# Kernel tuning notes

Measured on AMD Instinct MI355X. Metric: run time of the kernel, lower is better.

The kernel has to match this reference:

```python
import jax, jax.numpy as jnp
import numpy as np

INF = 1000000000000.0
V, H, E, B, T, S, NUM_OOV = 32000, 512, 300, 32, 32, 400, 50


def setup_inputs() -> dict:
    key = jax.random.key(0)
    ks = jax.random.split(key, 20)
    sc = 0.02
    inp = {
        'trg_seq_embedded': jax.random.normal(ks[0], (B, T, E), jnp.float32),
        'ext_src_seq': jax.random.randint(ks[1], (B, S), 0, V + NUM_OOV, jnp.int32),
        'init_states': jax.random.normal(ks[2], (1, B, H), jnp.float32),
        'encoder_outputs': jax.random.normal(ks[3], (B, S, H), jnp.float32),
        'encoder_mask': jax.random.randint(ks[4], (B, S), 0, 2, jnp.int32),
        # parameters (PyTorch Linear convention: y = x @ W.T + b)
        'W_enc': sc * jax.random.normal(ks[5], (H, H), jnp.float32),
        'b_enc': jnp.zeros((H,), jnp.float32),
        'W_red': sc * jax.random.normal(ks[6], (E, E + H), jnp.float32),
        'b_red': jnp.zeros((E,), jnp.float32),
        'W_ih': sc * jax.random.normal(ks[7], (4 * H, E), jnp.float32),
        'W_hh': sc * jax.random.normal(ks[8], (4 * H, H), jnp.float32),
        'b_ih': jnp.zeros((4 * H,), jnp.float32),
        'b_hh': jnp.zeros((4 * H,), jnp.float32),
        'W_cat': sc * jax.random.normal(ks[9], (H, 2 * H), jnp.float32),
        'b_cat': jnp.zeros((H,), jnp.float32),
        'W_log': sc * jax.random.normal(ks[10], (V, H), jnp.float32),
        'b_log': jnp.zeros((V,), jnp.float32),
    }
    return inp


def decoder_forward(trg_seq_embedded, init_states, encoder_outputs,
                    W_enc, b_enc, W_red, b_red, W_ih, W_hh, b_ih, b_hh,
                    W_cat, b_cat, W_log, b_log, ext_src_seq, encoder_mask):
    batch, max_len, _ = trg_seq_embedded.shape
    src_len = encoder_outputs.shape[1]
    hidden = encoder_outputs.shape[-1]
    memories = encoder_outputs @ W_enc.T + b_enc            # [B,S,H]
    mask0 = (encoder_mask == 0)                              # [B,S]
    bidx = jnp.arange(batch)[:, None]                        # [B,1]

    h0 = init_states[0]
    c0 = init_states[0]
    ctx0 = jnp.zeros((batch, hidden), trg_seq_embedded.dtype)
    cov0 = jnp.zeros((batch, src_len), trg_seq_embedded.dtype)

    def step(carry, emb_t):
        h, c, prev_ctx, cov = carry
        x = jnp.concatenate([emb_t, prev_ctx], axis=-1) @ W_red.T + b_red
        gates = x @ W_ih.T + b_ih + h @ W_hh.T + b_hh
        i, f, g, o = jnp.split(gates, 4, axis=-1)
        c_new = jax.nn.sigmoid(f) * c + jax.nn.sigmoid(i) * jnp.tanh(g)
        h_new = jax.nn.sigmoid(o) * jnp.tanh(c_new)
        energy = jnp.einsum('bh,bsh->bs', h_new, memories)
        energy = jnp.where(mask0, -INF, energy)
        attn = jax.nn.softmax(energy, axis=-1)
        ctx = jnp.einsum('bs,bsh->bh', attn, memories)
        logit_in = jnp.tanh(jnp.concatenate([h_new, ctx], axis=-1) @ W_cat.T + b_cat)
        logit = logit_in @ W_log.T + b_log                   # [B,V]
        ext = jnp.concatenate([logit, jnp.zeros((batch, NUM_OOV), logit.dtype)], axis=1)
        out = jnp.full_like(ext, -INF).at[bidx, ext_src_seq].max(energy)
        out = jnp.where(out == -INF, 0.0, out)
        logit_ext = ext + out
        logit_ext = jnp.where(logit_ext == 0.0, -INF, logit_ext)
        return (h_new, c_new, ctx, cov + attn), (logit_ext, attn, cov, energy)

    _, (logits, attns, covs, energies) = jax.lax.scan(
        step, (h0, c0, ctx0, cov0), jnp.swapaxes(trg_seq_embedded, 0, 1))
    return logits, attns, covs, energies


def reference(trg_seq_embedded, ext_src_seq, init_states, encoder_outputs, encoder_mask,
              W_enc, b_enc, W_red, b_red, W_ih, W_hh, b_ih, b_hh,
              W_cat, b_cat, W_log, b_log):
    return decoder_forward(trg_seq_embedded, init_states, encoder_outputs,
                           W_enc, b_enc, W_red, b_red, W_ih, W_hh, b_ih, b_hh,
                           W_cat, b_cat, W_log, b_log, ext_src_seq, encoder_mask)
```

## Files before the change

### kernel.cpp

```cpp
#include <hip/hip_runtime.h>
#include <hip/hip_bf16.h>

#define INF_F 1000000000000.0f

typedef __attribute__((ext_vector_type(8))) short bfrag8;
typedef __attribute__((ext_vector_type(4))) float facc4;
typedef __attribute__((ext_vector_type(4))) short short4v;

__device__ __forceinline__ float sigf(float x){ return 1.0f/(1.0f + expf(-x)); }
__device__ __forceinline__ short f2bf(float f){
  __hip_bfloat16 h = __float2bfloat16(f);
  return *reinterpret_cast<short*>(&h);
}
__device__ __forceinline__ float bf2f(short s){
  unsigned u = ((unsigned)(unsigned short)s) << 16;
  return *reinterpret_cast<float*>(&u);
}

#define OFF_LOG 0ull
#define OFF_A   32819200ull
#define OFF_C   33228800ull
#define OFF_E   33638400ull

__global__ __launch_bounds__(256) void k_init(const float* __restrict__ init_s,
    float* __restrict__ hbuf, float* __restrict__ c0, float* __restrict__ ctxb,
    float* __restrict__ cov) {
  int i = blockIdx.x*256 + threadIdx.x;
  if (i < 32*512) { float v = init_s[i]; hbuf[i]=v; c0[i]=v; ctxb[i]=0.0f; }
  if (i < 32*400) cov[i] = 0.0f;
}

__global__ __launch_bounds__(256) void k_bcombo(const float* __restrict__ W_ih,
    const float* __restrict__ b_red, const float* __restrict__ b_ih,
    const float* __restrict__ b_hh, float* __restrict__ bcomb) {
  int j = blockIdx.x*256 + threadIdx.x;
  if (j >= 2048) return;
  float acc = b_ih[j] + b_hh[j];
  for (int m=0;m<300;m++) acc += W_ih[j*300+m]*b_red[m];
  bcomb[j] = acc;
}

__global__ __launch_bounds__(256) void k_wcombo(const float* __restrict__ W_ih,
    const float* __restrict__ W_red, float* __restrict__ Wct) {
  __shared__ float As[16][68];
  __shared__ float Bs[16][68];
  int tid = threadIdx.x;
  int m0 = blockIdx.y*64, n0 = blockIdx.x*64;
  int rl = tid>>2, kq = (tid&3)*4;
  int kl = tid>>4, c4 = (tid&15)*4;
  int tx = tid&15, ty = tid>>4;
  float acc[4][4]={};
  for (int kk=0;kk<300;kk+=16){
    #pragma unroll
    for (int q=0;q<4;q++){
      int kg = kk+kq+q;
      As[kq+q][rl] = (kg<300) ? W_ih[(size_t)(m0+rl)*300 + kg] : 0.0f;
    }
    #pragma unroll
    for (int q=0;q<4;q++){
      int c = n0 + c4 + q;
      Bs[kl][c4+q] = (kk+kl<300 && c<812) ? W_red[(size_t)(kk+kl)*812 + c] : 0.0f;
    }
    __syncthreads();
    #pragma unroll
    for (int k=0;k<16;k++){
      const float* ap=&As[k][ty*4]; const float* bp=&Bs[k][tx*4];
      #pragma unroll
      for (int i=0;i<4;i++)
        #pragma unroll
        for (int j=0;j<4;j++) acc[i][j] += ap[i]*bp[j];
    }
    __syncthreads();
  }
  #pragma unroll
  for (int i=0;i<4;i++)
    #pragma unroll
    for (int j=0;j<4;j++){
      int row = m0+ty*4+i, col = n0+tx*4+j;
      if (col<812) Wct[(size_t)row*812 + col] = acc[i][j];
    }
}

__global__ __launch_bounds__(256) void k_gemb(const float* __restrict__ trg,
    const float* __restrict__ Wct, const float* __restrict__ bcomb,
    float* __restrict__ Gemb) {
  __shared__ float As[16][68];
  __shared__ float Bs[16][68];
  int tid = threadIdx.x;
  int m0 = blockIdx.y*64, n0 = blockIdx.x*64;
  int rl = tid>>2, kq = (tid&3)*4;
  int tx = tid&15, ty = tid>>4;
  float acc[4][4]={};
  int r = m0 + rl;
  const float* arow = trg + (size_t)(r&31)*9600 + (size_t)(r>>5)*300;
  for (int kk=0;kk<300;kk+=16){
    #pragma unroll
    for (int q=0;q<4;q++){
      int kg = kk+kq+q;
      As[kq+q][rl] = (kg<300) ? arow[kg] : 0.0f;
      Bs[kq+q][rl] = (kg<300) ? Wct[(size_t)(n0+rl)*812 + kg] : 0.0f;
    }
    __syncthreads();
    #pragma unroll
    for (int k=0;k<16;k++){
      const float* ap=&As[k][ty*4]; const float* bp=&Bs[k][tx*4];
      #pragma unroll
      for (int i=0;i<4;i++)
        #pragma unroll
        for (int j=0;j<4;j++) acc[i][j] += ap[i]*bp[j];
    }
    __syncthreads();
  }
  #pragma unroll
  for (int i=0;i<4;i++)
    #pragma unroll
    for (int j=0;j<4;j++){
      int rr = m0+ty*4+i, col = n0+tx*4+j;
      Gemb[(size_t)rr*2048 + col] = acc[i][j] + bcomb[col];
    }
}

__global__ __launch_bounds__(256) void k_wgpack(const float* __restrict__ Wct,
    const float* __restrict__ W_hh, float* __restrict__ Wg) {
  int idx = blockIdx.x*256 + threadIdx.x;
  if (idx >= 1024*2048) return;
  int k = idx >> 11, j = idx & 2047;
  Wg[idx] = (k < 512) ? Wct[(size_t)j*812 + 300 + k] : W_hh[(size_t)j*512 + (k-512)];
}

__global__ __launch_bounds__(256) void k_convsplit(const float* __restrict__ enc,
    const float* __restrict__ W_enc, short* __restrict__ ehi, short* __restrict__ elo,
    short* __restrict__ whi, short* __restrict__ wlo) {
  int i4 = blockIdx.x*256 + threadIdx.x;
  const float* src; short* dhi; short* dlo; size_t off;
  if (i4 < 1638400) { src = enc;   dhi = ehi; dlo = elo; off = (size_t)i4*4; }
  else { int j4 = i4 - 1638400; if (j4 >= 65536) return;
         src = W_enc; dhi = whi; dlo = wlo; off = (size_t)j4*4; }
  float4 v = *(const float4*)(src + off);
  float f[4] = {v.x, v.y, v.z, v.w};
  short4v h, l;
  #pragma unroll
  for (int q=0;q<4;q++){
    short hb = f2bf(f[q]);
    float r = f[q] - bf2f(hb);
    h[q] = hb; l[q] = f2bf(r);
  }
  *(short4v*)(dhi + off) = h;
  *(short4v*)(dlo + off) = l;
}

__device__ __forceinline__ int lds_off(int row, int slot) {
  return (row<<6) + (((slot ^ ((row>>1)&3))&3)<<4);
}

__global__ __launch_bounds__(256) void k_memories(const short* __restrict__ Ahg,
    const short* __restrict__ Alg, const short* __restrict__ Bhg,
    const short* __restrict__ Blg, const float* __restrict__ bias,
    float* __restrict__ mem) {
  __shared__ short Ah[4096];
  __shared__ short Al[4096];
  __shared__ short Bh[4096];
  __shared__ short Bl[4096];
  int tid = threadIdx.x;
  int m0 = blockIdx.x*128, n0 = blockIdx.y*128;
  int w = tid>>6, lane = tid&63;
  int wr = w>>1, wc = w&1;
  int lr = lane&15, kg2 = lane>>4;

  int srow = tid>>1;
  int ss   = (tid&1)*2;
  const short* gah = Ahg + (size_t)(m0+srow)*512 + ss*8;
  const short* gal = Alg + (size_t)(m0+srow)*512 + ss*8;
  const short* gbh = Bhg + (size_t)(n0+srow)*512 + ss*8;
  const short* gbl = Blg + (size_t)(n0+srow)*512 + ss*8;
  int wo0 = lds_off(srow, ss), wo1 = lds_off(srow, ss+1);

  int raoff[4], rboff[4];
  #pragma unroll
  for (int q=0;q<4;q++){
    raoff[q] = lds_off(wr*64 + q*16 + lr, kg2);
    rboff[q] = lds_off(wc*64 + q*16 + lr, kg2);
  }

  facc4 acc[4][4] = {};
  bfrag8 rah0 = *(const bfrag8*)(gah);
  bfrag8 rah1 = *(const bfrag8*)(gah+8);
  bfrag8 ral0 = *(const bfrag8*)(gal);
  bfrag8 ral1 = *(const bfrag8*)(gal+8);
  bfrag8 rbh0 = *(const bfrag8*)(gbh);
  bfrag8 rbh1 = *(const bfrag8*)(gbh+8);
  bfrag8 rbl0 = *(const bfrag8*)(gbl);
  bfrag8 rbl1 = *(const bfrag8*)(gbl+8);

  for (int i=0;i<16;i++){
    __syncthreads();
    *(bfrag8*)((char*)Ah + wo0) = rah0;
    *(bfrag8*)((char*)Ah + wo1) = rah1;
    *(bfrag8*)((char*)Al + wo0) = ral0;
    *(bfrag8*)((char*)Al + wo1) = ral1;
    *(bfrag8*)((char*)Bh + wo0) = rbh0;
    *(bfrag8*)((char*)Bh + wo1) = rbh1;
    *(bfrag8*)((char*)Bl + wo0) = rbl0;
    *(bfrag8*)((char*)Bl + wo1) = rbl1;
    __syncthreads();
    if (i<15){
      gah += 32; gal += 32; gbh += 32; gbl += 32;
      rah0 = *(const bfrag8*)(gah);
      rah1 = *(const bfrag8*)(gah+8);
      ral0 = *(const bfrag8*)(gal);
      ral1 = *(const bfrag8*)(gal+8);
      rbh0 = *(const bfrag8*)(gbh);
      rbh1 = *(const bfrag8*)(gbh+8);
      rbl0 = *(const bfrag8*)(gbl);
      rbl1 = *(const bfrag8*)(gbl+8);
    }
    bfrag8 afh[4], afl[4], bfh[4], bfl[4];
    #pragma unroll
    for (int q=0;q<4;q++){
      afh[q] = *(const bfrag8*)((char*)Ah + raoff[q]);
      afl[q] = *(const bfrag8*)((char*)Al + raoff[q]);
      bfh[q] = *(const bfrag8*)((char*)Bh + rboff[q]);
      bfl[q] = *(const bfrag8*)((char*)Bl + rboff[q]);
    }
    #pragma unroll
    for (int mi=0;mi<4;mi++)
      #pragma unroll
      for (int ni=0;ni<4;ni++){
        acc[mi][ni] = __builtin_amdgcn_mfma_f32_16x16x32_bf16(afl[mi], bfh[ni], acc[mi][ni], 0,0,0);
        acc[mi][ni] = __builtin_amdgcn_mfma_f32_16x16x32_bf16(afh[mi], bfl[ni], acc[mi][ni], 0,0,0);
        acc[mi][ni] = __builtin_amdgcn_mfma_f32_16x16x32_bf16(afh[mi], bfh[ni], acc[mi][ni], 0,0,0);
      }
  }

  #pragma unroll
  for (int mi=0;mi<4;mi++){
    int row = m0 + wr*64 + mi*16 + kg2*4;
    #pragma unroll
    for (int ni=0;ni<4;ni++){
      int col = n0 + wc*64 + ni*16 + lr;
      float bl = bias[col];
      #pragma unroll
      for (int q=0;q<4;q++)
        mem[(size_t)(row+q)*512 + col] = acc[mi][ni][q] + bl;
    }
  }
}

__global__ __launch_bounds__(256) void k_wlogconv(const float* __restrict__ W_log,
    __hip_bfloat16* __restrict__ wlb, const float* __restrict__ W_cat,
    short* __restrict__ wcatb) {
  int i4 = blockIdx.x*256 + threadIdx.x;
  if (i4 < 4096000) {
    const float4 v = *(const float4*)(W_log + (size_t)i4*4);
    size_t o = (size_t)i4*4;
    wlb[o+0] = __float2bfloat16(v.x); wlb[o+1] = __float2bfloat16(v.y);
    wlb[o+2] = __float2bfloat16(v.z); wlb[o+3] = __float2bfloat16(v.w);
  } else {
    int j4 = i4 - 4096000;
    if (j4 >= 131072) return;
    const float4 v = *(const float4*)(W_cat + (size_t)j4*4);
    short4v s;
    s[0]=f2bf(v.x); s[1]=f2bf(v.y); s[2]=f2bf(v.z); s[3]=f2bf(v.w);
    *(short4v*)(wcatb + (size_t)j4*4) = s;
  }
}

__global__ __launch_bounds__(512) void k_gates(const float* __restrict__ ctxb,
    const float* __restrict__ hbuf, const float* __restrict__ Wg,
    float* __restrict__ partials) {
  __shared__ float yh_s[64][32];
  int ks = blockIdx.x;
  int rc = blockIdx.y;
  int tid = threadIdx.x;
  const float* side = (ks < 8) ? ctxb : hbuf;
  int kbase = (ks & 7) * 64;
  {
    int b_l = tid & 31, kq0 = (tid >> 5) * 4;
    const float* src = side + (size_t)b_l*512 + kbase + kq0;
    float4 v = *(const float4*)src;
    yh_s[kq0+0][b_l]=v.x; yh_s[kq0+1][b_l]=v.y;
    yh_s[kq0+2][b_l]=v.z; yh_s[kq0+3][b_l]=v.w;
  }
  __syncthreads();
  int tr = tid & 63, bg = tid >> 6;
  int row0 = rc*128 + tr*2;
  float acc[2][4] = {};
  const float* wp = Wg + (size_t)(ks*64)*2048 + row0;
  #pragma unroll 8
  for (int k=0;k<64;k++){
    float2 w = *(const float2*)(wp + (size_t)k*2048);
    float4 y = *(const float4*)&yh_s[k][bg*4];
    acc[0][0]+=w.x*y.x; acc[0][1]+=w.x*y.y; acc[0][2]+=w.x*y.z; acc[0][3]+=w.x*y.w;
    acc[1][0]+=w.y*y.x; acc[1][1]+=w.y*y.y; acc[1][2]+=w.y*y.z; acc[1][3]+=w.y*y.w;
  }
  #pragma unroll
  for (int j=0;j<4;j++){
    float2 o; o.x=acc[0][j]; o.y=acc[1][j];
    *(float2*)(partials + (size_t)(ks*32 + bg*4 + j)*2048 + row0) = o;
  }
}

__global__ __launch_bounds__(512) void k_lstm_energy(const float* __restrict__ part,
    const float* __restrict__ Gemb,
    const float* __restrict__ c_in, float* __restrict__ c_out,
    float* __restrict__ hbuf, short* __restrict__ licat,
    const float* __restrict__ mem, const int* __restrict__ emask,
    float* __restrict__ out, int t) {
  __shared__ float hl[512];
  int blk = blockIdx.x, tid = threadIdx.x;
  int b = blk & 31, sc = blk >> 5;
  int r = t*32 + b;
  int lane = tid & 63, w = tid >> 6;
  {
    int j = tid;
    const float* gp = Gemb + (size_t)r*2048;
    float g[4];
    #pragma unroll
    for (int gi=0; gi<4; gi++){
      int row = gi*512 + j;
      float v = gp[row];
      #pragma unroll
      for (int ks=0; ks<16; ks++)
        v += part[(size_t)(ks*32+b)*2048 + row];
      g[gi] = v;
    }
    float cp = c_in[b*512+j];
    float cn = sigf(g[1])*cp + sigf(g[0])*tanhf(g[2]);
    float hn = sigf(g[3])*tanhf(cn);
    hl[j] = hn;
    if (sc==0){
      c_out[b*512+j]=cn; hbuf[b*512+j]=hn;
      licat[(size_t)r*1024 + j] = f2bf(hn);
    }
  }
  __syncthreads();
  float4 h0 = *(const float4*)&hl[lane*8];
  float4 h1 = *(const float4*)&hl[lane*8+4];
  const float* mb = mem + (size_t)b*204800;
  const int* em = emask + b*400;
  for (int i=0;i<7;i++){
    int s_l = i*8 + w;
    if (s_l < 50){
      int s = sc*50 + s_l;
      const float4* mp = (const float4*)(mb + (size_t)s*512 + lane*8);
      float4 m0 = mp[0], m1 = mp[1];
      float acc = h0.x*m0.x + h0.y*m0.y + h0.z*m0.z + h0.w*m0.w
                + h1.x*m1.x + h1.y*m1.y + h1.z*m1.z + h1.w*m1.w;
      #pragma unroll
      for (int off=32; off; off>>=1) acc += __shfl_xor(acc, off);
      if (lane==0){
        out[OFF_E + (size_t)r*400 + s] = (em[s]==0) ? -INF_F : acc;
      }
    }
  }
}

__global__ __launch_bounds__(512) void k_ctx(float* __restrict__ out,
    const float* __restrict__ mem, float* __restrict__ ctxb, short* __restrict__ licat,
    float* __restrict__ cov, int t) {
  __shared__ float ps[400];
  __shared__ float red[16];
  __shared__ float tmp[512];
  int blk = blockIdx.x, tid = threadIdx.x;
  int b = blk & 31, hc = blk >> 5;
  int r = t*32 + b;
  int lane = tid & 63, w = tid >> 6;
  float e = (tid < 400) ? out[OFF_E + (size_t)r*400 + tid] : -3.4e38f;
  float lm = e;
  #pragma unroll
  for (int off=32; off; off>>=1) lm = fmaxf(lm, __shfl_xor(lm, off));
  if (lane==0) red[w] = lm;
  __syncthreads();
  float m = red[0];
  #pragma unroll
  for (int i=1;i<8;i++) m = fmaxf(m, red[i]);
  float pv = (tid < 400) ? expf(e - m) : 0.0f;
  float sv = pv;
  #pragma unroll
  for (int off=32; off; off>>=1) sv += __shfl_xor(sv, off);
  if (lane==0) red[8+w] = sv;
  __syncthreads();
  float sum = red[8];
  #pragma unroll
  for (int i=1;i<8;i++) sum += red[8+i];
  float inv = 1.0f/sum;
  if (tid < 400) ps[tid] = pv*inv;
  __syncthreads();
  int hloc = tid & 63, sh = tid >> 6;
  int h = hc*64 + hloc;
  float acc = 0.0f;
  {
    const float* mqs = mem + (size_t)b*204800 + h + (size_t)sh*50*512;
    const float* pss = &ps[sh*50];
    #pragma unroll 10
    for (int s=0;s<50;s++) acc += pss[s]*mqs[(size_t)s*512];
  }
  tmp[sh*64 + hloc] = acc;
  __syncthreads();
  if (sh==0){
    float v = acc;
    #pragma unroll
    for (int q=1;q<8;q++) v += tmp[q*64 + hloc];
    ctxb[b*512+h] = v;
    licat[(size_t)r*1024 + 512 + h] = f2bf(v);
  }
  if (hc==0 && tid<400){
    float a = ps[tid];
    out[OFF_A + (size_t)r*400 + tid] = a;
    float cv = cov[b*400+tid];
    out[OFF_C + (size_t)r*400 + tid] = cv;
    cov[b*400+tid] = cv + a;
  }
}

__global__ __launch_bounds__(256) void k_logitin(const short* __restrict__ Ab,
    const short* __restrict__ Wb, const float* __restrict__ b_cat,
    __hip_bfloat16* __restrict__ lib) {
  __shared__ short As[4096];
  __shared__ short Bs[4096];
  int tid = threadIdx.x;
  int m0 = blockIdx.x*128, n0 = blockIdx.y*128;
  int w = tid>>6, lane = tid&63;
  int wr = w>>1, wc = w&1;
  int lr = lane&15, kg2 = lane>>4;

  int srow = tid>>1;
  int ss   = (tid&1)*2;
  const short* ga = Ab + (size_t)(m0+srow)*1024 + ss*8;
  const short* gw = Wb + (size_t)(n0+srow)*1024 + ss*8;
  int wo0 = lds_off(srow, ss), wo1 = lds_off(srow, ss+1);

  int raoff[4], rboff[4];
  #pragma unroll
  for (int q=0;q<4;q++){
    raoff[q] = lds_off(wr*64 + q*16 + lr, kg2);
    rboff[q] = lds_off(wc*64 + q*16 + lr, kg2);
  }

  facc4 acc[4][4] = {};
  bfrag8 ra0 = *(const bfrag8*)(ga);
  bfrag8 ra1 = *(const bfrag8*)(ga+8);
  bfrag8 rb0 = *(const bfrag8*)(gw);
  bfrag8 rb1 = *(const bfrag8*)(gw+8);

  for (int i=0;i<32;i++){
    __syncthreads();
    *(bfrag8*)((char*)As + wo0) = ra0;
    *(bfrag8*)((char*)As + wo1) = ra1;
    *(bfrag8*)((char*)Bs + wo0) = rb0;
    *(bfrag8*)((char*)Bs + wo1) = rb1;
    __syncthreads();
    if (i<31){
      ga += 32; gw += 32;
      ra0 = *(const bfrag8*)(ga);
      ra1 = *(const bfrag8*)(ga+8);
      rb0 = *(const bfrag8*)(gw);
      rb1 = *(const bfrag8*)(gw+8);
    }
    bfrag8 af[4], bf[4];
    #pragma unroll
    for (int q=0;q<4;q++){
      af[q] = *(const bfrag8*)((char*)As + raoff[q]);
      bf[q] = *(const bfrag8*)((char*)Bs + rboff[q]);
    }
    #pragma unroll
    for (int mi=0;mi<4;mi++)
      #pragma unroll
      for (int ni=0;ni<4;ni++)
        acc[mi][ni] = __builtin_amdgcn_mfma_f32_16x16x32_bf16(af[mi], bf[ni], acc[mi][ni], 0,0,0);
  }

  #pragma unroll
  for (int mi=0;mi<4;mi++){
    int row = m0 + wr*64 + mi*16 + kg2*4;
    #pragma unroll
    for (int ni=0;ni<4;ni++){
      int col = n0 + wc*64 + ni*16 + lr;
      float bc = b_cat[col];
      #pragma unroll
      for (int q=0;q<4;q++){
        float v = tanhf(acc[mi][ni][q] + bc);
        lib[(size_t)(row+q)*512 + col] = __float2bfloat16(v);
      }
    }
  }
}

__global__ __launch_bounds__(256) void k_logits(const __hip_bfloat16* __restrict__ Ab,
    const __hip_bfloat16* __restrict__ Wb, const float* __restrict__ b_log,
    float* __restrict__ out) {
  __shared__ short As[4096];
  __shared__ short Bs[4096];
  int m = blockIdx.y & 7;
  int yy = blockIdx.x + 8*(blockIdx.y >> 3);
  if (yy >= 250) return;
  int tid = threadIdx.x;
  int m0 = m*128, n0 = yy*128;
  int w = tid>>6, lane = tid&63;
  int wr = w>>1, wc = w&1;
  int lr = lane&15, kg2 = lane>>4;
  const short* A = (const short*)Ab;
  const short* W = (const short*)Wb;

  int srow = tid>>1;
  int ss   = (tid&1)*2;
  const short* ga = A + (size_t)(m0+srow)*512 + ss*8;
  const short* gw = W + (size_t)(n0+srow)*512 + ss*8;
  int wo0 = lds_off(srow, ss), wo1 = lds_off(srow, ss+1);

  int raoff[4], rboff[4];
  #pragma unroll
  for (int q=0;q<4;q++){
    raoff[q] = lds_off(wr*64 + q*16 + lr, kg2);
    rboff[q] = lds_off(wc*64 + q*16 + lr, kg2);
  }

  facc4 acc[4][4] = {};
  bfrag8 ra0 = *(const bfrag8*)(ga);
  bfrag8 ra1 = *(const bfrag8*)(ga+8);
  bfrag8 rb0 = *(const bfrag8*)(gw);
  bfrag8 rb1 = *(const bfrag8*)(gw+8);

  for (int i=0;i<16;i++){
    __syncthreads();
    *(bfrag8*)((char*)As + wo0) = ra0;
    *(bfrag8*)((char*)As + wo1) = ra1;
    *(bfrag8*)((char*)Bs + wo0) = rb0;
    *(bfrag8*)((char*)Bs + wo1) = rb1;
    __syncthreads();
    if (i<15){
      ga += 32; gw += 32;
      ra0 = *(const bfrag8*)(ga);
      ra1 = *(const bfrag8*)(ga+8);
      rb0 = *(const bfrag8*)(gw);
      rb1 = *(const bfrag8*)(gw+8);
    }
    bfrag8 af[4], bf[4];
    #pragma unroll
    for (int q=0;q<4;q++){
      af[q] = *(const bfrag8*)((char*)As + raoff[q]);
      bf[q] = *(const bfrag8*)((char*)Bs + rboff[q]);
    }
    #pragma unroll
    for (int mi=0;mi<4;mi++)
      #pragma unroll
      for (int ni=0;ni<4;ni++)
        acc[mi][ni] = __builtin_amdgcn_mfma_f32_16x16x32_bf16(af[mi], bf[ni], acc[mi][ni], 0,0,0);
  }

  #pragma unroll
  for (int mi=0;mi<4;mi++){
    int row = m0 + wr*64 + mi*16 + kg2*4;
    #pragma unroll
    for (int ni=0;ni<4;ni++){
      int col = n0 + wc*64 + ni*16 + lr;
      float bl = b_log[col];
      #pragma unroll
      for (int q=0;q<4;q++){
        float v = acc[mi][ni][q] + bl;
        out[(size_t)(row+q)*32050 + col] = (v == 0.0f) ? -INF_F : v;
      }
    }
  }
}

__global__ __launch_bounds__(512) void k_scatter(const int* __restrict__ ext_src,
    float* __restrict__ out) {
  __shared__ int tok[400];
  __shared__ float ev[400];
  int rr = blockIdx.x;
  int b = rr & 31;
  int tid = threadIdx.x;
  if (tid >= 400 && tid < 450)
    out[(size_t)rr*32050 + 32000 + (tid-400)] = -INF_F;
  if (tid < 400){
    tok[tid] = ext_src[b*400+tid];
    ev[tid]  = out[OFF_E + (size_t)rr*400 + tid];
  }
  __syncthreads();
  if (tid < 400){
    int tk = tok[tid];
    float m = -3.4e38f;
    bool pre = false;
    #pragma unroll 1
    for (int s2=0; s2<400; s2+=8){
      #pragma unroll
      for (int q=0;q<8;q++){
        int tk2 = tok[s2+q];
        float e2 = ev[s2+q];
        bool eq = (tk2==tk);
        m = fmaxf(m, eq ? e2 : -3.4e38f);
        pre = pre || (eq && (s2+q) < tid);
      }
    }
    if (!pre && m != -INF_F){
      size_t idx = (size_t)rr*32050 + tk;
      float wv = out[idx];
      float extv = (wv == -INF_F) ? 0.0f : wv;
      float nv = extv + m;
      out[idx] = (nv == 0.0f) ? -INF_F : nv;
    }
  }
}

extern "C" void kernel_launch(void* const* d_in, const int* in_sizes, int n_in,
                              void* d_out, int out_size, void* d_ws, size_t ws_size,
                              hipStream_t stream) {
  const float* trg   = (const float*)d_in[0];
  const int*   ext   = (const int*)  d_in[1];
  const float* inits = (const float*)d_in[2];
  const float* enc   = (const float*)d_in[3];
  const int*   emask = (const int*)  d_in[4];
  const float* W_enc = (const float*)d_in[5];
  const float* b_enc = (const float*)d_in[6];
  const float* W_red = (const float*)d_in[7];
  const float* b_red = (const float*)d_in[8];
  const float* W_ih  = (const float*)d_in[9];
  const float* W_hh  = (const float*)d_in[10];
  const float* b_ih  = (const float*)d_in[11];
  const float* b_hh  = (const float*)d_in[12];
  const float* W_cat = (const float*)d_in[13];
  const float* b_cat = (const float*)d_in[14];
  const float* W_log = (const float*)d_in[15];
  const float* b_log = (const float*)d_in[16];
  float* out = (float*)d_out;
  float* ws  = (float*)d_ws;

  float* mem   = ws + 0ull;
  float* Wg    = ws + 6553600ull;
  float* Wct   = ws + 8650752ull;
  float* Gemb  = ws + 10313728ull;
  float* bcomb = ws + 12410880ull;
  float* hbuf  = ws + 12412928ull;
  float* c0    = ws + 12429312ull;
  float* c1    = ws + 12445696ull;
  float* ctxb  = ws + 12462080ull;
  float* cov   = ws + 13527040ull;
  float* part  = ws + 13539840ull;
  __hip_bfloat16* lib = (__hip_bfloat16*)(ws + 14590464ull);
  short* licat = (short*)(ws + 8650752ull);
  short* wcatb = (short*)(ws + 9175040ull);
  __hip_bfloat16* wlb = (__hip_bfloat16*)(ws + 15245824ull);
  short* ehi = (short*)(ws + 15245824ull);
  short* elo = ehi + 6553600;
  short* whi = ehi + 13107200;
  short* wlo = ehi + 13369344;

  k_init<<<64,256,0,stream>>>(inits, hbuf, c0, ctxb, cov);
  k_bcombo<<<8,256,0,stream>>>(W_ih, b_red, b_ih, b_hh, bcomb);
  k_wcombo<<<dim3(13,32),256,0,stream>>>(W_ih, W_red, Wct);
  k_gemb<<<dim3(32,16),256,0,stream>>>(trg, Wct, bcomb, Gemb);
  k_wgpack<<<8192,256,0,stream>>>(Wct, W_hh, Wg);
  k_convsplit<<<6656,256,0,stream>>>(enc, W_enc, ehi, elo, whi, wlo);
  k_memories<<<dim3(100,4),256,0,stream>>>(ehi, elo, whi, wlo, b_enc, mem);
  k_wlogconv<<<16512,256,0,stream>>>(W_log, wlb, W_cat, wcatb);

  for (int t=0;t<32;t++){
    const float* c_in = (t&1) ? c1 : c0;
    float* c_out      = (t&1) ? c0 : c1;
    k_gates<<<dim3(16,16),512,0,stream>>>(ctxb, hbuf, Wg, part);
    k_lstm_energy<<<256,512,0,stream>>>(part, Gemb, c_in, c_out, hbuf, licat,
                                        mem, emask, out, t);
    k_ctx<<<256,512,0,stream>>>(out, mem, ctxb, licat, cov, t);
  }

  k_logitin<<<dim3(8,4),256,0,stream>>>(licat, wcatb, b_cat, lib);
  k_logits<<<dim3(8,256),256,0,stream>>>(lib, wlb, b_log, out);
  k_scatter<<<1024,512,0,stream>>>(ext, out);
}
```

Before: 950.0 us.

## Merge prep kernels into one launch and reshape gate GEMV split-K

Folds the weight-pack, encoder split-convert and W_log/W_cat bf16 conversion kernels into a single k_prep launch. To allow that, W_log's bf16 copy moves to a separate workspace region so it no longer aliases the encoder hi/lo buffers. The per-step gate GEMV goes from 16 k-slices of 64 to 8 k-slices of 128, with one row per thread, which halves the partial sums that the LSTM kernel must reduce. The intent is fewer launches and less partial-sum traffic, at the cost of a longer serial k-loop per thread and a larger workspace footprint.

```diff
diff --git a/kernel.cpp b/kernel.cpp
--- a/kernel.cpp
+++ b/kernel.cpp
@@ -120,33 +120,51 @@
     }
 }
 
-__global__ __launch_bounds__(256) void k_wgpack(const float* __restrict__ Wct,
-    const float* __restrict__ W_hh, float* __restrict__ Wg) {
-  int idx = blockIdx.x*256 + threadIdx.x;
-  if (idx >= 1024*2048) return;
-  int k = idx >> 11, j = idx & 2047;
-  Wg[idx] = (k < 512) ? Wct[(size_t)j*812 + 300 + k] : W_hh[(size_t)j*512 + (k-512)];
-}
-
-__global__ __launch_bounds__(256) void k_convsplit(const float* __restrict__ enc,
-    const float* __restrict__ W_enc, short* __restrict__ ehi, short* __restrict__ elo,
-    short* __restrict__ whi, short* __restrict__ wlo) {
-  int i4 = blockIdx.x*256 + threadIdx.x;
-  const float* src; short* dhi; short* dlo; size_t off;
-  if (i4 < 1638400) { src = enc;   dhi = ehi; dlo = elo; off = (size_t)i4*4; }
-  else { int j4 = i4 - 1638400; if (j4 >= 65536) return;
-         src = W_enc; dhi = whi; dlo = wlo; off = (size_t)j4*4; }
-  float4 v = *(const float4*)(src + off);
-  float f[4] = {v.x, v.y, v.z, v.w};
-  short4v h, l;
-  #pragma unroll
-  for (int q=0;q<4;q++){
-    short hb = f2bf(f[q]);
-    float r = f[q] - bf2f(hb);
-    h[q] = hb; l[q] = f2bf(r);
-  }
-  *(short4v*)(dhi + off) = h;
-  *(short4v*)(dlo + off) = l;
+__global__ __launch_bounds__(256) void k_prep(const float* __restrict__ Wct,
+    const float* __restrict__ W_hh, float* __restrict__ Wg,
+    const float* __restrict__ enc, const float* __restrict__ W_enc,
+    short* __restrict__ ehi, short* __restrict__ elo,
+    short* __restrict__ whi, short* __restrict__ wlo,
+    const float* __restrict__ W_log, __hip_bfloat16* __restrict__ wlb,
+    const float* __restrict__ W_cat, short* __restrict__ wcatb) {
+  int bx = blockIdx.x;
+  if (bx < 8192) {
+    int idx = bx*256 + threadIdx.x;
+    int k = idx >> 11, j = idx & 2047;
+    Wg[idx] = (k < 512) ? Wct[(size_t)j*812 + 300 + k] : W_hh[(size_t)j*512 + (k-512)];
+  } else if (bx < 14848) {
+    int i4 = (bx-8192)*256 + threadIdx.x;
+    const float* src; short* dhi; short* dlo; size_t off;
+    if (i4 < 1638400) { src = enc;   dhi = ehi; dlo = elo; off = (size_t)i4*4; }
+    else { int j4 = i4 - 1638400; if (j4 >= 65536) return;
+           src = W_enc; dhi = whi; dlo = wlo; off = (size_t)j4*4; }
+    float4 v = *(const float4*)(src + off);
+    float f[4] = {v.x, v.y, v.z, v.w};
+    short4v h, l;
+    #pragma unroll
+    for (int q=0;q<4;q++){
+      short hb = f2bf(f[q]);
+      float rr = f[q] - bf2f(hb);
+      h[q] = hb; l[q] = f2bf(rr);
+    }
+    *(short4v*)(dhi + off) = h;
+    *(short4v*)(dlo + off) = l;
+  } else {
+    int i4 = (bx-14848)*256 + threadIdx.x;
+    if (i4 < 4096000) {
+      const float4 v = *(const float4*)(W_log + (size_t)i4*4);
+      size_t o = (size_t)i4*4;
+      wlb[o+0] = __float2bfloat16(v.x); wlb[o+1] = __float2bfloat16(v.y);
+      wlb[o+2] = __float2bfloat16(v.z); wlb[o+3] = __float2bfloat16(v.w);
+    } else {
+      int j4 = i4 - 4096000;
+      if (j4 >= 131072) return;
+      const float4 v = *(const float4*)(W_cat + (size_t)j4*4);
+      short4v s;
+      s[0]=f2bf(v.x); s[1]=f2bf(v.y); s[2]=f2bf(v.z); s[3]=f2bf(v.w);
+      *(short4v*)(wcatb + (size_t)j4*4) = s;
+    }
+  }
 }
 
 __device__ __forceinline__ int lds_off(int row, int slot) {
@@ -246,58 +264,39 @@
   }
 }
 
-__global__ __launch_bounds__(256) void k_wlogconv(const float* __restrict__ W_log,
-    __hip_bfloat16* __restrict__ wlb, const float* __restrict__ W_cat,
-    short* __restrict__ wcatb) {
-  int i4 = blockIdx.x*256 + threadIdx.x;
-  if (i4 < 4096000) {
-    const float4 v = *(const float4*)(W_log + (size_t)i4*4);
-    size_t o = (size_t)i4*4;
-    wlb[o+0] = __float2bfloat16(v.x); wlb[o+1] = __float2bfloat16(v.y);
-    wlb[o+2] = __float2bfloat16(v.z); wlb[o+3] = __float2bfloat16(v.w);
-  } else {
-    int j4 = i4 - 4096000;
-    if (j4 >= 131072) return;
-    const float4 v = *(const float4*)(W_cat + (size_t)j4*4);
-    short4v s;
-    s[0]=f2bf(v.x); s[1]=f2bf(v.y); s[2]=f2bf(v.z); s[3]=f2bf(v.w);
-    *(short4v*)(wcatb + (size_t)j4*4) = s;
-  }
-}
-
 __global__ __launch_bounds__(512) void k_gates(const float* __restrict__ ctxb,
     const float* __restrict__ hbuf, const float* __restrict__ Wg,
     float* __restrict__ partials) {
-  __shared__ float yh_s[64][32];
+  __shared__ float yh_s[128][32];
   int ks = blockIdx.x;
   int rc = blockIdx.y;
   int tid = threadIdx.x;
-  const float* side = (ks < 8) ? ctxb : hbuf;
-  int kbase = (ks & 7) * 64;
+  const float* side = (ks < 4) ? ctxb : hbuf;
+  int kbase = (ks & 3) * 128;
   {
-    int b_l = tid & 31, kq0 = (tid >> 5) * 4;
+    int b_l = tid >> 4, kq0 = (tid & 15) * 8;
     const float* src = side + (size_t)b_l*512 + kbase + kq0;
-    float4 v = *(const float4*)src;
-    yh_s[kq0+0][b_l]=v.x; yh_s[kq0+1][b_l]=v.y;
-    yh_s[kq0+2][b_l]=v.z; yh_s[kq0+3][b_l]=v.w;
+    float4 v0 = *(const float4*)(src);
+    float4 v1 = *(const float4*)(src + 4);
+    yh_s[kq0+0][b_l]=v0.x; yh_s[kq0+1][b_l]=v0.y;
+    yh_s[kq0+2][b_l]=v0.z; yh_s[kq0+3][b_l]=v0.w;
+    yh_s[kq0+4][b_l]=v1.x; yh_s[kq0+5][b_l]=v1.y;
+    yh_s[kq0+6][b_l]=v1.z; yh_s[kq0+7][b_l]=v1.w;
   }
   __syncthreads();
   int tr = tid & 63, bg = tid >> 6;
-  int row0 = rc*128 + tr*2;
-  float acc[2][4] = {};
-  const float* wp = Wg + (size_t)(ks*64)*2048 + row0;
+  int row = rc*64 + tr;
+  float acc[4] = {};
+  const float* wp = Wg + (size_t)(ks*128)*2048 + row;
   #pragma unroll 8
-  for (int k=0;k<64;k++){
-    float2 w = *(const float2*)(wp + (size_t)k*2048);
+  for (int k=0;k<128;k++){
+    float w = wp[(size_t)k*2048];
     float4 y = *(const float4*)&yh_s[k][bg*4];
-    acc[0][0]+=w.x*y.x; acc[0][1]+=w.x*y.y; acc[0][2]+=w.x*y.z; acc[0][3]+=w.x*y.w;
-    acc[1][0]+=w.y*y.x; acc[1][1]+=w.y*y.y; acc[1][2]+=w.y*y.z; acc[1][3]+=w.y*y.w;
-  }
-  #pragma unroll
-  for (int j=0;j<4;j++){
-    float2 o; o.x=acc[0][j]; o.y=acc[1][j];
-    *(float2*)(partials + (size_t)(ks*32 + bg*4 + j)*2048 + row0) = o;
-  }
+    acc[0]+=w*y.x; acc[1]+=w*y.y; acc[2]+=w*y.z; acc[3]+=w*y.w;
+  }
+  #pragma unroll
+  for (int j=0;j<4;j++)
+    partials[(size_t)(ks*32 + bg*4 + j)*2048 + row] = acc[j];
 }
 
 __global__ __launch_bounds__(512) void k_lstm_energy(const float* __restrict__ part,
@@ -320,7 +319,7 @@
       int row = gi*512 + j;
       float v = gp[row];
       #pragma unroll
-      for (int ks=0; ks<16; ks++)
+      for (int ks=0; ks<8; ks++)
         v += part[(size_t)(ks*32+b)*2048 + row];
       g[gi] = v;
     }
@@ -645,26 +644,26 @@
   short* elo = ehi + 6553600;
   short* whi = ehi + 13107200;
   short* wlo = ehi + 13369344;
+  __hip_bfloat16* wlb2 = (__hip_bfloat16*)(ws + 22076416ull);
 
   k_init<<<64,256,0,stream>>>(inits, hbuf, c0, ctxb, cov);
   k_bcombo<<<8,256,0,stream>>>(W_ih, b_red, b_ih, b_hh, bcomb);
   k_wcombo<<<dim3(13,32),256,0,stream>>>(W_ih, W_red, Wct);
   k_gemb<<<dim3(32,16),256,0,stream>>>(trg, Wct, bcomb, Gemb);
-  k_wgpack<<<8192,256,0,stream>>>(Wct, W_hh, Wg);
-  k_convsplit<<<6656,256,0,stream>>>(enc, W_enc, ehi, elo, whi, wlo);
+  k_prep<<<31360,256,0,stream>>>(Wct, W_hh, Wg, enc, W_enc, ehi, elo, whi, wlo,
+                                 W_log, wlb2, W_cat, wcatb);
   k_memories<<<dim3(100,4),256,0,stream>>>(ehi, elo, whi, wlo, b_enc, mem);
-  k_wlogconv<<<16512,256,0,stream>>>(W_log, wlb, W_cat, wcatb);
 
   for (int t=0;t<32;t++){
     const float* c_in = (t&1) ? c1 : c0;
     float* c_out      = (t&1) ? c0 : c1;
-    k_gates<<<dim3(16,16),512,0,stream>>>(ctxb, hbuf, Wg, part);
+    k_gates<<<dim3(8,32),512,0,stream>>>(ctxb, hbuf, Wg, part);
     k_lstm_energy<<<256,512,0,stream>>>(part, Gemb, c_in, c_out, hbuf, licat,
                                         mem, emask, out, t);
     k_ctx<<<256,512,0,stream>>>(out, mem, ctxb, licat, cov, t);
   }
 
   k_logitin<<<dim3(8,4),256,0,stream>>>(licat, wcatb, b_cat, lib);
-  k_logits<<<dim3(8,256),256,0,stream>>>(lib, wlb, b_log, out);
+  k_logits<<<dim3(8,256),256,0,stream>>>(lib, wlb2, b_log, out);
   k_scatter<<<1024,512,0,stream>>>(ext, out);
 }
```

Result: slower. 1.007 ms (+6.0%).
